# Kernel tuning notes

Measured on AMD Instinct MI355X. Metric: run time of the kernel, lower is better.

Reference implementation:

```python
import jax, jax.numpy as jnp
import numpy as np

B, S, F_IN, E, H, NIT = 256, 196, 384, 384, 8, 10
FH = E                      # hidden_features defaults to embed_dim
EH = E // H                 # embed dim per head = 48
FHH = FH // H               # hidden features per head = 48
OSEQ = S                    # hidden_seq_len defaults to seq_len
MIN_POS = 1e-6
W_THRESH = 1e-5


def _l1(x, axis=-1, eps=1e-12):
    # F.normalize(p=1): x / max(sum|x|, eps)
    return x / jnp.clip(jnp.sum(jnp.abs(x), axis=axis, keepdims=True), eps, None)


def _norm_weight(w):
    # normalize_weights(): L1-normalize, clamp at threshold, L1-normalize again
    w = _l1(w, axis=-1)
    w = jnp.clip(w, W_THRESH, None)
    return _l1(w, axis=-1)


def setup_inputs() -> dict:
    key = jax.random.key(0)
    ks = jax.random.split(key, 7)
    x = jax.random.normal(ks[0], (B, S, F_IN), dtype=jnp.float32)
    # h init: torch.rand in _reset_h (uniform positive)
    h0 = jax.random.uniform(ks[1], (B, OSEQ, H, FHH), dtype=jnp.float32)
    embed_w = jax.random.normal(ks[2], (E, F_IN), dtype=jnp.float32) * 0.05
    embed_b = jnp.zeros((E,), dtype=jnp.float32)
    local_weight = _norm_weight(jax.random.uniform(ks[3], (FHH, EH), dtype=jnp.float32))
    global_weight = _norm_weight(jax.random.uniform(ks[4], (H, OSEQ, S), dtype=jnp.float32))
    out_w = jax.random.normal(ks[5], (F_IN, E), dtype=jnp.float32) * 0.05
    out_b = jnp.zeros((F_IN,), dtype=jnp.float32)
    return {"x": x, "h0": h0, "embed_w": embed_w, "embed_b": embed_b,
            "local_weight": local_weight, "global_weight": global_weight,
            "out_w": out_w, "out_b": out_b}


def reference(x, h0, embed_w, embed_b, local_weight, global_weight, out_w, out_b):
    # embed + clamp + split heads: [B,S,H,EH]
    xe = jnp.clip(x @ embed_w.T + embed_b, MIN_POS, None)
    xe = xe.reshape(B, S, H, EH)
    # _prepare_input: L1 normalize over last dim (eps=1e-20); nonneg so |x|=x
    inp = xe / jnp.clip(jnp.sum(xe, axis=-1, keepdims=True), 1e-20, None)
    # h init, L1-normalized
    h = _l1(h0, axis=-1)

    def nnmf_forward(t):  # t: [B,S(=i),H,EH]
        t = jnp.einsum('bihe,fe->bihf', t, local_weight)          # F.linear(x, local_weight)
        return jnp.einsum('bihf,hoi->bohf', t, global_weight)     # [B,O,H,FHH]

    def nnmf_reconstruct(hh):  # hh: [B,O,H,FHH]
        t = jnp.einsum('bohf,hoi->bihf', hh, global_weight)
        return jnp.einsum('bihf,fe->bihe', t, local_weight)       # F.linear(., local_weight.t())

    # fixed-point NNMF iterations (h_update_rate=1)
    for _ in range(NIT):
        rec = jnp.clip(nnmf_reconstruct(h), MIN_POS, None)   # secure tensor
        rec = _l1(rec, axis=-1)                              # normalize_reconstruction
        h = h * nnmf_forward(inp / rec)                      # multiplicative update
        h = jnp.clip(h, MIN_POS, None)                       # _secure_tensor
        h = h / jnp.sum(h, axis=-1, keepdims=True)           # PowerSoftmax(power=1)

    # output = 'hidden': flatten heads, project back to features
    out = h.reshape(B, OSEQ, FH)
    return out @ out_w.T + out_b
```

## Files before the change

### kernel.cpp

```cpp
#include <hip/hip_runtime.h>
#include <stdint.h>

#define NB   256
#define NS   196
#define NF   384
#define NH   8
#define NEH  48
#define NIT  10
#define SP   224
#define EP   64
#define NBH  2048
#define NBS  50176
#define NT   13

using f32x4  = __attribute__((ext_vector_type(4))) float;
using u16x8  = __attribute__((ext_vector_type(8))) uint16_t;
using u16x4  = __attribute__((ext_vector_type(4))) uint16_t;
using bf16x8 = __attribute__((ext_vector_type(8))) __bf16;

static __device__ __forceinline__ float bf2f(uint16_t u){
  union { uint32_t u32; float f; } c; c.u32 = (uint32_t)u << 16; return c.f;
}
static __device__ __forceinline__ uint16_t f2bf(float f){
  __bf16 h = (__bf16)f;
  return __builtin_bit_cast(uint16_t, h);
}
static __device__ __forceinline__ float frcp(float f){
  return __builtin_amdgcn_rcpf(f);
}
static __device__ __forceinline__ bf16x8 ld8(const uint16_t* p){
  return __builtin_bit_cast(bf16x8, *(const u16x8*)p);
}
static __device__ __forceinline__ void lds_fence(){
  asm volatile("s_waitcnt lgkmcnt(0)" ::: "memory");
}
static __device__ __forceinline__ float dpp_add16(float x){
  int v = __builtin_bit_cast(int, x);
  x += __builtin_bit_cast(float, __builtin_amdgcn_update_dpp(0, v, 0xB1, 0xF, 0xF, false));
  v = __builtin_bit_cast(int, x);
  x += __builtin_bit_cast(float, __builtin_amdgcn_update_dpp(0, v, 0x4E, 0xF, 0xF, false));
  v = __builtin_bit_cast(int, x);
  x += __builtin_bit_cast(float, __builtin_amdgcn_update_dpp(0, v, 0x141, 0xF, 0xF, false));
  v = __builtin_bit_cast(int, x);
  x += __builtin_bit_cast(float, __builtin_amdgcn_update_dpp(0, v, 0x140, 0xF, 0xF, false));
  return x;
}
#define MFMA16(a,b,c) __builtin_amdgcn_mfma_f32_16x16x32_bf16((a),(b),(c),0,0,0)


__global__ void k_prep_gw(const float* __restrict__ gw, uint16_t* __restrict__ gw_b,
                          uint16_t* __restrict__ gwt_b){
  int idx = blockIdx.x * 256 + threadIdx.x;
  if (idx >= NH*SP*SP) return;
  int h = idx / (SP*SP);
  int r = (idx / SP) % SP;
  int c = idx % SP;
  float v = (r < NS && c < NS) ? gw[((size_t)h*NS + r)*NS + c] : 0.f;
  uint16_t bv = f2bf(v);
  gw_b[idx] = bv;
  gwt_b[((size_t)h*SP + c)*SP + r] = bv;
}

__global__ void k_prep_small(const float* __restrict__ lw, const float* __restrict__ ew,
                             const float* __restrict__ ow,
                             uint16_t* __restrict__ lw_b, uint16_t* __restrict__ lwt_b,
                             uint16_t* __restrict__ ew_b, uint16_t* __restrict__ ow_b){
  int idx = blockIdx.x * 256 + threadIdx.x;
  if (idx < EP*EP){
    int f = idx >> 6, e = idx & 63;
    float v = (f < NEH && e < NEH) ? lw[f*NEH + e] : 0.f;
    uint16_t bv = f2bf(v);
    lw_b[f*EP + e] = bv;
    lwt_b[e*EP + f] = bv;
  }
  if (idx < NF*NF){
    ew_b[idx] = f2bf(ew[idx]);
    ow_b[idx] = f2bf(ow[idx]);
  }
}

__global__ __launch_bounds__(512) void k_embed(const float* __restrict__ x,
    const uint16_t* __restrict__ ew_b, const float* __restrict__ eb,
    uint16_t* __restrict__ inp_fm){
  const int wave = threadIdx.x >> 6, lane = threadIdx.x & 63;
  const int lg = lane >> 4, li = lane & 15;
  const int mt = wave >> 1, nh = wave & 1;
  const int m0 = blockIdx.x * 64 + mt * 16;
  f32x4 acc[12];
  #pragma unroll
  for (int i = 0; i < 12; ++i) acc[i] = (f32x4)0.0f;
  const float* ap = x + (size_t)(m0 + li) * NF + 8*lg;
  for (int kt = 0; kt < 12; ++kt){
    f32x4 a0 = *(const f32x4*)(ap + kt*32);
    f32x4 a1 = *(const f32x4*)(ap + kt*32 + 4);
    u16x8 au;
    #pragma unroll
    for (int j = 0; j < 4; ++j){ au[j] = f2bf(a0[j]); au[j+4] = f2bf(a1[j]); }
    bf16x8 a = __builtin_bit_cast(bf16x8, au);
    #pragma unroll
    for (int nt = 0; nt < 12; ++nt){
      bf16x8 b = ld8(ew_b + (size_t)((nh*12 + nt)*16 + li)*NF + kt*32 + 8*lg);
      acc[nt] = MFMA16(a, b, acc[nt]);
    }
  }
  #pragma unroll
  for (int hl = 0; hl < 4; ++hl){
    int hh = nh*4 + hl;
    float xec[3][4];
    float s[4] = {0.f, 0.f, 0.f, 0.f};
    #pragma unroll
    for (int j = 0; j < 3; ++j){
      int nt = hl*3 + j;
      float bias = eb[(nh*12 + nt)*16 + li];
      #pragma unroll
      for (int r = 0; r < 4; ++r){
        float v = fmaxf(acc[nt][r] + bias, 1e-6f);
        xec[j][r] = v; s[r] += v;
      }
    }
    #pragma unroll
    for (int r = 0; r < 4; ++r) s[r] = dpp_add16(s[r]);
    #pragma unroll
    for (int r = 0; r < 4; ++r){
      int m = m0 + 4*lg + r;
      int b = m / NS, si = m - b*NS;
      int t = si >> 4, wi = si & 15;
      int lanep = (wi >> 2)*16 + li;
      float inv = frcp(s[r]);
      size_t base = ((size_t)((b*NH + hh)*NT + t)*64 + lanep)*12 + (wi & 3);
      #pragma unroll
      for (int j = 0; j < 3; ++j)
        inp_fm[base + j*4] = f2bf(xec[j][r] * inv);
    }
  }
}

__global__ __launch_bounds__(448) void k_main(
    const float*    __restrict__ h0,
    const uint16_t* __restrict__ gw_b,
    const uint16_t* __restrict__ gwt_b,
    const uint16_t* __restrict__ lw_b,
    const uint16_t* __restrict__ lwt_b,
    const uint16_t* __restrict__ inp_fm,
    uint16_t* __restrict__ h_b)
{
  __shared__ __align__(16) uint16_t hlT[48][232];
  __shared__ __align__(16) uint16_t t2T[48][232];
  __shared__ __align__(16) uint16_t Sg[7][2][16][72];

  const int bh = blockIdx.x;
  const int b  = bh >> 3;
  const int hh = bh & 7;
  const int tid = threadIdx.x;
  const int wave = tid >> 6;
  const int lane = tid & 63;
  const int lg = lane >> 4;
  const int li = lane & 15;
  const int tt[2] = {wave, wave + 7};

  {
    u16x4 z = {0,0,0,0};
    *(u16x4*)&Sg[wave][0][li][48 + 4*lg] = z;
    *(u16x4*)&Sg[wave][1][li][48 + 4*lg] = z;
  }

  bf16x8 lwtF[3][2], lwF[3][2];
  #pragma unroll
  for (int nt = 0; nt < 3; ++nt)
    #pragma unroll
    for (int kt = 0; kt < 2; ++kt){
      lwtF[nt][kt] = ld8(lwt_b + (size_t)(nt*16 + li)*EP + kt*32 + 8*lg);
      lwF [nt][kt] = ld8(lw_b  + (size_t)(nt*16 + li)*EP + kt*32 + 8*lg);
    }

  u16x4 ip[2][3];
  #pragma unroll
  for (int tp = 0; tp < 2; ++tp){
    const int t = tt[tp];
    if (t < NT){
      const uint16_t* ipp = inp_fm + ((size_t)(bh*NT + t)*64 + lg*16 + li)*12;
      ip[tp][0] = *(const u16x4*)(ipp);
      ip[tp][1] = *(const u16x4*)(ipp + 4);
      ip[tp][2] = *(const u16x4*)(ipp + 8);
    } else {
      u16x4 z = {0,0,0,0};
      ip[tp][0] = z; ip[tp][1] = z; ip[tp][2] = z;
    }
  }

  float hr[2][3][4];
  #pragma unroll
  for (int tp = 0; tp < 2; ++tp){
    const int t = tt[tp];
    float s[4] = {0.f,0.f,0.f,0.f};
    #pragma unroll
    for (int nt = 0; nt < 3; ++nt)
      #pragma unroll
      for (int r = 0; r < 4; ++r){
        int row = t*16 + 4*lg + r;
        float v = 0.f;
        if (row < NS)
          v = h0[(((size_t)(b*NS + row))*NH + hh)*NEH + nt*16 + li];
        hr[tp][nt][r] = v;
        s[r] += fabsf(v);
      }
    #pragma unroll
    for (int r = 0; r < 4; ++r) s[r] = frcp(fmaxf(dpp_add16(s[r]), 1e-12f));
    #pragma unroll
    for (int nt = 0; nt < 3; ++nt)
      #pragma unroll
      for (int r = 0; r < 4; ++r){
        hr[tp][nt][r] *= s[r];
        Sg[wave][tp][4*lg + r][nt*16 + li] = f2bf(hr[tp][nt][r]);
      }
  }
  lds_fence();
  #pragma unroll
  for (int tp = 0; tp < 2; ++tp){
    const int t = tt[tp];
    f32x4 hl[3];
    #pragma unroll
    for (int i = 0; i < 3; ++i) hl[i] = (f32x4)0.0f;
    #pragma unroll
    for (int kt = 0; kt < 2; ++kt){
      bf16x8 a = ld8(&Sg[wave][tp][li][kt*32 + 8*lg]);
      #pragma unroll
      for (int nt = 0; nt < 3; ++nt) hl[nt] = MFMA16(a, lwtF[nt][kt], hl[nt]);
    }
    #pragma unroll
    for (int nt = 0; nt < 3; ++nt){
      u16x4 w;
      #pragma unroll
      for (int r = 0; r < 4; ++r) w[r] = f2bf(hl[nt][r]);
      *(u16x4*)&hlT[nt*16 + li][t*16 + 4*lg] = w;
    }
  }

  const uint16_t* __restrict__ gwh  = gw_b  + (size_t)hh * SP * SP;
  const uint16_t* __restrict__ gwth = gwt_b + (size_t)hh * SP * SP;
  const uint16_t* gA0t = gwth + (size_t)(tt[0]*16 + li)*SP + 8*lg;
  const uint16_t* gA1t = gwth + (size_t)(tt[1]*16 + li)*SP + 8*lg;
  const uint16_t* gA0  = gwh  + (size_t)(tt[0]*16 + li)*SP + 8*lg;
  const uint16_t* gA1  = gwh  + (size_t)(tt[1]*16 + li)*SP + 8*lg;
  __syncthreads();

  for (int it = 0; it < NIT; ++it){
    f32x4 rec[2][3];
    #pragma unroll
    for (int tp = 0; tp < 2; ++tp)
      #pragma unroll
      for (int i = 0; i < 3; ++i) rec[tp][i] = (f32x4)0.0f;
    #pragma unroll
    for (int kt = 0; kt < 7; ++kt){
      bf16x8 b0 = ld8(&hlT[ 0 + li][kt*32 + 8*lg]);
      bf16x8 b1 = ld8(&hlT[16 + li][kt*32 + 8*lg]);
      bf16x8 b2 = ld8(&hlT[32 + li][kt*32 + 8*lg]);
      bf16x8 a0 = ld8(gA0t + kt*32);
      bf16x8 a1 = ld8(gA1t + kt*32);
      rec[0][0] = MFMA16(a0, b0, rec[0][0]);
      rec[0][1] = MFMA16(a0, b1, rec[0][1]);
      rec[0][2] = MFMA16(a0, b2, rec[0][2]);
      rec[1][0] = MFMA16(a1, b0, rec[1][0]);
      rec[1][1] = MFMA16(a1, b1, rec[1][1]);
      rec[1][2] = MFMA16(a1, b2, rec[1][2]);
    }
    #pragma unroll
    for (int tp = 0; tp < 2; ++tp){
      float s[4] = {0.f,0.f,0.f,0.f};
      float rv[3][4];
      #pragma unroll
      for (int nt = 0; nt < 3; ++nt)
        #pragma unroll
        for (int r = 0; r < 4; ++r){
          float v = fmaxf(rec[tp][nt][r], 1e-6f);
          rv[nt][r] = v; s[r] += v;
        }
      #pragma unroll
      for (int r = 0; r < 4; ++r) s[r] = dpp_add16(s[r]);
      #pragma unroll
      for (int r = 0; r < 4; ++r){
        Sg[wave][tp][4*lg + r][ 0 + li] = f2bf(bf2f(ip[tp][0][r]) * s[r] * frcp(rv[0][r]));
        Sg[wave][tp][4*lg + r][16 + li] = f2bf(bf2f(ip[tp][1][r]) * s[r] * frcp(rv[1][r]));
        Sg[wave][tp][4*lg + r][32 + li] = f2bf(bf2f(ip[tp][2][r]) * s[r] * frcp(rv[2][r]));
      }
    }
    lds_fence();
    #pragma unroll
    for (int tp = 0; tp < 2; ++tp){
      const int t = tt[tp];
      f32x4 t2[3];
      #pragma unroll
      for (int i = 0; i < 3; ++i) t2[i] = (f32x4)0.0f;
      #pragma unroll
      for (int kt = 0; kt < 2; ++kt){
        bf16x8 a = ld8(&Sg[wave][tp][li][kt*32 + 8*lg]);
        #pragma unroll
        for (int nt = 0; nt < 3; ++nt) t2[nt] = MFMA16(a, lwF[nt][kt], t2[nt]);
      }
      #pragma unroll
      for (int nt = 0; nt < 3; ++nt){
        u16x4 w;
        #pragma unroll
        for (int r = 0; r < 4; ++r) w[r] = f2bf(t2[nt][r]);
        *(u16x4*)&t2T[nt*16 + li][t*16 + 4*lg] = w;
      }
    }
    __syncthreads();

    f32x4 hu[2][3];
    #pragma unroll
    for (int tp = 0; tp < 2; ++tp)
      #pragma unroll
      for (int i = 0; i < 3; ++i) hu[tp][i] = (f32x4)0.0f;
    #pragma unroll
    for (int kt = 0; kt < 7; ++kt){
      bf16x8 b0 = ld8(&t2T[ 0 + li][kt*32 + 8*lg]);
      bf16x8 b1 = ld8(&t2T[16 + li][kt*32 + 8*lg]);
      bf16x8 b2 = ld8(&t2T[32 + li][kt*32 + 8*lg]);
      bf16x8 a0 = ld8(gA0 + kt*32);
      bf16x8 a1 = ld8(gA1 + kt*32);
      hu[0][0] = MFMA16(a0, b0, hu[0][0]);
      hu[0][1] = MFMA16(a0, b1, hu[0][1]);
      hu[0][2] = MFMA16(a0, b2, hu[0][2]);
      hu[1][0] = MFMA16(a1, b0, hu[1][0]);
      hu[1][1] = MFMA16(a1, b1, hu[1][1]);
      hu[1][2] = MFMA16(a1, b2, hu[1][2]);
    }
    #pragma unroll
    for (int tp = 0; tp < 2; ++tp){
      float s[4] = {0.f,0.f,0.f,0.f};
      #pragma unroll
      for (int nt = 0; nt < 3; ++nt)
        #pragma unroll
        for (int r = 0; r < 4; ++r){
          float v = fmaxf(hr[tp][nt][r] * hu[tp][nt][r], 1e-6f);
          hr[tp][nt][r] = v; s[r] += v;
        }
      #pragma unroll
      for (int r = 0; r < 4; ++r) s[r] = frcp(dpp_add16(s[r]));
      #pragma unroll
      for (int nt = 0; nt < 3; ++nt)
        #pragma unroll
        for (int r = 0; r < 4; ++r){
          hr[tp][nt][r] *= s[r];
          Sg[wave][tp][4*lg + r][nt*16 + li] = f2bf(hr[tp][nt][r]);
        }
    }
    lds_fence();
    #pragma unroll
    for (int tp = 0; tp < 2; ++tp){
      const int t = tt[tp];
      f32x4 hl[3];
      #pragma unroll
      for (int i = 0; i < 3; ++i) hl[i] = (f32x4)0.0f;
      #pragma unroll
      for (int kt = 0; kt < 2; ++kt){
        bf16x8 a = ld8(&Sg[wave][tp][li][kt*32 + 8*lg]);
        #pragma unroll
        for (int nt = 0; nt < 3; ++nt) hl[nt] = MFMA16(a, lwtF[nt][kt], hl[nt]);
      }
      #pragma unroll
      for (int nt = 0; nt < 3; ++nt){
        u16x4 w;
        #pragma unroll
        for (int r = 0; r < 4; ++r) w[r] = f2bf(hl[nt][r]);
        *(u16x4*)&hlT[nt*16 + li][t*16 + 4*lg] = w;
      }
    }
    __syncthreads();
  }

  uint16_t* __restrict__ hrow = h_b + (size_t)bh * SP * EP;
  #pragma unroll
  for (int tp = 0; tp < 2; ++tp){
    const int t = tt[tp];
    #pragma unroll
    for (int nt = 0; nt < 3; ++nt)
      #pragma unroll
      for (int r = 0; r < 4; ++r){
        int row = t*16 + 4*lg + r;
        if (row < NS)
          hrow[(size_t)row*EP + nt*16 + li] = f2bf(hr[tp][nt][r]);
      }
  }
}

__global__ __launch_bounds__(512) void k_out(const uint16_t* __restrict__ h_b,
    const uint16_t* __restrict__ ow_b, const float* __restrict__ obv,
    float* __restrict__ out){
  const int wave = threadIdx.x >> 6, lane = threadIdx.x & 63;
  const int lg = lane >> 4, li = lane & 15;
  const int mt = wave >> 1, nh = wave & 1;
  const int m0 = blockIdx.x * 64 + mt * 16;
  const int m = m0 + li;
  const int b = m / NS, si = m - b*NS;
  f32x4 acc[12];
  #pragma unroll
  for (int i = 0; i < 12; ++i) acc[i] = (f32x4)0.0f;
  for (int kt = 0; kt < 12; ++kt){
    int ks = kt*32 + 8*lg;
    int hh = ks / NEH, f = ks - hh*NEH;
    bf16x8 a = ld8(h_b + ((size_t)(b*NH + hh)*SP + si)*EP + f);
    #pragma unroll
    for (int nt = 0; nt < 12; ++nt){
      bf16x8 bb = ld8(ow_b + (size_t)((nh*12 + nt)*16 + li)*NF + kt*32 + 8*lg);
      acc[nt] = MFMA16(a, bb, acc[nt]);
    }
  }
  #pragma unroll
  for (int nt = 0; nt < 12; ++nt){
    float bias = obv[(nh*12 + nt)*16 + li];
    #pragma unroll
    for (int r = 0; r < 4; ++r)
      out[(size_t)(m0 + 4*lg + r)*NF + (nh*12 + nt)*16 + li] = acc[nt][r] + bias;
  }
}

extern "C" void kernel_launch(void* const* d_in, const int* in_sizes, int n_in,
                              void* d_out, int out_size, void* d_ws, size_t ws_size,
                              hipStream_t stream){
  const float* x   = (const float*)d_in[0];
  const float* h0  = (const float*)d_in[1];
  const float* ew  = (const float*)d_in[2];
  const float* eb  = (const float*)d_in[3];
  const float* lw  = (const float*)d_in[4];
  const float* gw  = (const float*)d_in[5];
  const float* ow  = (const float*)d_in[6];
  const float* obv = (const float*)d_in[7];
  float* out = (float*)d_out;

  char* w = (char*)d_ws;
  size_t o_inp = 0;
  size_t o_hb  = o_inp + (size_t)NBH*NT*64*12*2;
  size_t o_gw  = o_hb  + (size_t)NBH*SP*EP*2;
  size_t o_gwt = o_gw  + (size_t)NH*SP*SP*2;
  size_t o_lw  = o_gwt + (size_t)NH*SP*SP*2;
  size_t o_lwt = o_lw  + (size_t)EP*EP*2;
  size_t o_ew  = o_lwt + (size_t)EP*EP*2;
  size_t o_ow  = o_ew  + (size_t)NF*NF*2;
  size_t total = o_ow  + (size_t)NF*NF*2;
  if (ws_size < total) return;

  uint16_t* inp_fm = (uint16_t*)(w + o_inp);
  uint16_t* h_b    = (uint16_t*)(w + o_hb);
  uint16_t* gw_b   = (uint16_t*)(w + o_gw);
  uint16_t* gwt_b  = (uint16_t*)(w + o_gwt);
  uint16_t* lw_b   = (uint16_t*)(w + o_lw);
  uint16_t* lwt_b  = (uint16_t*)(w + o_lwt);
  uint16_t* ew_b   = (uint16_t*)(w + o_ew);
  uint16_t* ow_b   = (uint16_t*)(w + o_ow);

  k_prep_gw<<<(NH*SP*SP + 255)/256, 256, 0, stream>>>(gw, gw_b, gwt_b);
  k_prep_small<<<(NF*NF + 255)/256, 256, 0, stream>>>(lw, ew, ow, lw_b, lwt_b, ew_b, ow_b);
  k_embed<<<NBS/64, 512, 0, stream>>>(x, ew_b, eb, inp_fm);
  k_main<<<NBH, 448, 0, stream>>>(h0, gw_b, gwt_b, lw_b, lwt_b, inp_fm, h_b);
  k_out<<<NBS/64, 512, 0, stream>>>(h_b, ow_b, obv, out);
}
```

Baseline: 735.4 us.

## Rebalance NNMF tiles across 8 waves, vectorize embed stores, retile output GEMM

The main kernel moves from 7 waves with two tiles each to 8 waves, where waves 0-5 handle two tiles and waves 6-7 handle one, with shared staging indexed by tile. This spreads the 13 tiles over more waves to shorten the per-wave critical path, at the cost of divergent branching on ntile. The embed kernel now hoists the index math and writes four packed bf16 values per store instead of scalar stores. The output GEMM gives each wave two M-tiles by six N-tiles so each B fragment load feeds two MFMAs.

```diff
diff --git a/kernel.cpp b/kernel.cpp
--- a/kernel.cpp
+++ b/kernel.cpp
@@ -103,6 +103,11 @@
       acc[nt] = MFMA16(a, b, acc[nt]);
     }
   }
+  const int mbase = m0 + 4*lg;
+  const int b  = mbase / NS;
+  const int si = mbase - b*NS;
+  const int t  = si >> 4, wi = si & 15;
+  const int lanep = (wi >> 2)*16 + li;
   #pragma unroll
   for (int hl = 0; hl < 4; ++hl){
     int hh = nh*4 + hl;
@@ -119,23 +124,19 @@
       }
     }
     #pragma unroll
-    for (int r = 0; r < 4; ++r) s[r] = dpp_add16(s[r]);
-    #pragma unroll
-    for (int r = 0; r < 4; ++r){
-      int m = m0 + 4*lg + r;
-      int b = m / NS, si = m - b*NS;
-      int t = si >> 4, wi = si & 15;
-      int lanep = (wi >> 2)*16 + li;
-      float inv = frcp(s[r]);
-      size_t base = ((size_t)((b*NH + hh)*NT + t)*64 + lanep)*12 + (wi & 3);
-      #pragma unroll
-      for (int j = 0; j < 3; ++j)
-        inp_fm[base + j*4] = f2bf(xec[j][r] * inv);
-    }
-  }
-}
-
-__global__ __launch_bounds__(448) void k_main(
+    for (int r = 0; r < 4; ++r) s[r] = frcp(dpp_add16(s[r]));
+    uint16_t* dst = inp_fm + ((size_t)((b*NH + hh)*NT + t)*64 + lanep)*12;
+    #pragma unroll
+    for (int j = 0; j < 3; ++j){
+      u16x4 w;
+      #pragma unroll
+      for (int r = 0; r < 4; ++r) w[r] = f2bf(xec[j][r] * s[r]);
+      *(u16x4*)(dst + j*4) = w;
+    }
+  }
+}
+
+__global__ __launch_bounds__(512) void k_main(
     const float*    __restrict__ h0,
     const uint16_t* __restrict__ gw_b,
     const uint16_t* __restrict__ gwt_b,
@@ -146,7 +147,7 @@
 {
   __shared__ __align__(16) uint16_t hlT[48][232];
   __shared__ __align__(16) uint16_t t2T[48][232];
-  __shared__ __align__(16) uint16_t Sg[7][2][16][72];
+  __shared__ __align__(16) uint16_t Sg[14][16][72];
 
   const int bh = blockIdx.x;
   const int b  = bh >> 3;
@@ -156,12 +157,14 @@
   const int lane = tid & 63;
   const int lg = lane >> 4;
   const int li = lane & 15;
-  const int tt[2] = {wave, wave + 7};
+  const int ntile = (wave < 6) ? 2 : 1;
+  const int tt[2] = {wave, wave + 8};
 
   {
     u16x4 z = {0,0,0,0};
-    *(u16x4*)&Sg[wave][0][li][48 + 4*lg] = z;
-    *(u16x4*)&Sg[wave][1][li][48 + 4*lg] = z;
+    #pragma unroll
+    for (int tp = 0; tp < 2; ++tp)
+      if (tp < ntile) *(u16x4*)&Sg[tt[tp]][li][48 + 4*lg] = z;
   }
 
   bf16x8 lwtF[3][2], lwF[3][2];
@@ -176,72 +179,78 @@
   u16x4 ip[2][3];
   #pragma unroll
   for (int tp = 0; tp < 2; ++tp){
-    const int t = tt[tp];
-    if (t < NT){
-      const uint16_t* ipp = inp_fm + ((size_t)(bh*NT + t)*64 + lg*16 + li)*12;
+    u16x4 z = {0,0,0,0};
+    ip[tp][0] = z; ip[tp][1] = z; ip[tp][2] = z;
+    if (tp < ntile && tt[tp] < NT){
+      const uint16_t* ipp = inp_fm + ((size_t)(bh*NT + tt[tp])*64 + lg*16 + li)*12;
       ip[tp][0] = *(const u16x4*)(ipp);
       ip[tp][1] = *(const u16x4*)(ipp + 4);
       ip[tp][2] = *(const u16x4*)(ipp + 8);
-    } else {
-      u16x4 z = {0,0,0,0};
-      ip[tp][0] = z; ip[tp][1] = z; ip[tp][2] = z;
     }
   }
 
   float hr[2][3][4];
   #pragma unroll
   for (int tp = 0; tp < 2; ++tp){
-    const int t = tt[tp];
-    float s[4] = {0.f,0.f,0.f,0.f};
-    #pragma unroll
-    for (int nt = 0; nt < 3; ++nt)
-      #pragma unroll
-      for (int r = 0; r < 4; ++r){
-        int row = t*16 + 4*lg + r;
-        float v = 0.f;
-        if (row < NS)
-          v = h0[(((size_t)(b*NS + row))*NH + hh)*NEH + nt*16 + li];
-        hr[tp][nt][r] = v;
-        s[r] += fabsf(v);
-      }
-    #pragma unroll
-    for (int r = 0; r < 4; ++r) s[r] = frcp(fmaxf(dpp_add16(s[r]), 1e-12f));
-    #pragma unroll
-    for (int nt = 0; nt < 3; ++nt)
-      #pragma unroll
-      for (int r = 0; r < 4; ++r){
-        hr[tp][nt][r] *= s[r];
-        Sg[wave][tp][4*lg + r][nt*16 + li] = f2bf(hr[tp][nt][r]);
-      }
+    if (tp < ntile){
+      const int t = tt[tp];
+      float s[4] = {0.f,0.f,0.f,0.f};
+      #pragma unroll
+      for (int nt = 0; nt < 3; ++nt)
+        #pragma unroll
+        for (int r = 0; r < 4; ++r){
+          int row = t*16 + 4*lg + r;
+          float v = 0.f;
+          if (row < NS)
+            v = h0[(((size_t)(b*NS + row))*NH + hh)*NEH + nt*16 + li];
+          hr[tp][nt][r] = v;
+          s[r] += fabsf(v);
+        }
+      #pragma unroll
+      for (int r = 0; r < 4; ++r) s[r] = frcp(fmaxf(dpp_add16(s[r]), 1e-12f));
+      #pragma unroll
+      for (int nt = 0; nt < 3; ++nt)
+        #pragma unroll
+        for (int r = 0; r < 4; ++r){
+          hr[tp][nt][r] *= s[r];
+          Sg[t][4*lg + r][nt*16 + li] = f2bf(hr[tp][nt][r]);
+        }
+    }
   }
   lds_fence();
   #pragma unroll
   for (int tp = 0; tp < 2; ++tp){
-    const int t = tt[tp];
-    f32x4 hl[3];
-    #pragma unroll
-    for (int i = 0; i < 3; ++i) hl[i] = (f32x4)0.0f;
-    #pragma unroll
-    for (int kt = 0; kt < 2; ++kt){
-      bf16x8 a = ld8(&Sg[wave][tp][li][kt*32 + 8*lg]);
-      #pragma unroll
-      for (int nt = 0; nt < 3; ++nt) hl[nt] = MFMA16(a, lwtF[nt][kt], hl[nt]);
-    }
-    #pragma unroll
-    for (int nt = 0; nt < 3; ++nt){
-      u16x4 w;
-      #pragma unroll
-      for (int r = 0; r < 4; ++r) w[r] = f2bf(hl[nt][r]);
-      *(u16x4*)&hlT[nt*16 + li][t*16 + 4*lg] = w;
+    if (tp < ntile){
+      const int t = tt[tp];
+      f32x4 hl[3];
+      #pragma unroll
+      for (int i = 0; i < 3; ++i) hl[i] = (f32x4)0.0f;
+      #pragma unroll
+      for (int kt = 0; kt < 2; ++kt){
+        bf16x8 a = ld8(&Sg[t][li][kt*32 + 8*lg]);
+        #pragma unroll
+        for (int nt = 0; nt < 3; ++nt) hl[nt] = MFMA16(a, lwtF[nt][kt], hl[nt]);
+      }
+      #pragma unroll
+      for (int nt = 0; nt < 3; ++nt){
+        u16x4 w;
+        #pragma unroll
+        for (int r = 0; r < 4; ++r) w[r] = f2bf(hl[nt][r]);
+        *(u16x4*)&hlT[nt*16 + li][t*16 + 4*lg] = w;
+      }
     }
   }
 
   const uint16_t* __restrict__ gwh  = gw_b  + (size_t)hh * SP * SP;
   const uint16_t* __restrict__ gwth = gwt_b + (size_t)hh * SP * SP;
   const uint16_t* gA0t = gwth + (size_t)(tt[0]*16 + li)*SP + 8*lg;
-  const uint16_t* gA1t = gwth + (size_t)(tt[1]*16 + li)*SP + 8*lg;
+  const uint16_t* gA1t = gwth + (size_t)(tt[0]*16 + li)*SP + 8*lg;
   const uint16_t* gA0  = gwh  + (size_t)(tt[0]*16 + li)*SP + 8*lg;
-  const uint16_t* gA1  = gwh  + (size_t)(tt[1]*16 + li)*SP + 8*lg;
+  const uint16_t* gA1  = gA0;
+  if (ntile == 2){
+    gA1t = gwth + (size_t)(tt[1]*16 + li)*SP + 8*lg;
+    gA1  = gwh  + (size_t)(tt[1]*16 + li)*SP + 8*lg;
+  }
   __syncthreads();
 
   for (int it = 0; it < NIT; ++it){
@@ -256,53 +265,60 @@
       bf16x8 b1 = ld8(&hlT[16 + li][kt*32 + 8*lg]);
       bf16x8 b2 = ld8(&hlT[32 + li][kt*32 + 8*lg]);
       bf16x8 a0 = ld8(gA0t + kt*32);
-      bf16x8 a1 = ld8(gA1t + kt*32);
       rec[0][0] = MFMA16(a0, b0, rec[0][0]);
       rec[0][1] = MFMA16(a0, b1, rec[0][1]);
       rec[0][2] = MFMA16(a0, b2, rec[0][2]);
-      rec[1][0] = MFMA16(a1, b0, rec[1][0]);
-      rec[1][1] = MFMA16(a1, b1, rec[1][1]);
-      rec[1][2] = MFMA16(a1, b2, rec[1][2]);
+      if (ntile == 2){
+        bf16x8 a1 = ld8(gA1t + kt*32);
+        rec[1][0] = MFMA16(a1, b0, rec[1][0]);
+        rec[1][1] = MFMA16(a1, b1, rec[1][1]);
+        rec[1][2] = MFMA16(a1, b2, rec[1][2]);
+      }
     }
     #pragma unroll
     for (int tp = 0; tp < 2; ++tp){
-      float s[4] = {0.f,0.f,0.f,0.f};
-      float rv[3][4];
-      #pragma unroll
-      for (int nt = 0; nt < 3; ++nt)
+      if (tp < ntile){
+        const int t = tt[tp];
+        float s[4] = {0.f,0.f,0.f,0.f};
+        float rv[3][4];
+        #pragma unroll
+        for (int nt = 0; nt < 3; ++nt)
+          #pragma unroll
+          for (int r = 0; r < 4; ++r){
+            float v = fmaxf(rec[tp][nt][r], 1e-6f);
+            rv[nt][r] = v; s[r] += v;
+          }
+        #pragma unroll
+        for (int r = 0; r < 4; ++r) s[r] = dpp_add16(s[r]);
         #pragma unroll
         for (int r = 0; r < 4; ++r){
-          float v = fmaxf(rec[tp][nt][r], 1e-6f);
-          rv[nt][r] = v; s[r] += v;
-        }
-      #pragma unroll
-      for (int r = 0; r < 4; ++r) s[r] = dpp_add16(s[r]);
-      #pragma unroll
-      for (int r = 0; r < 4; ++r){
-        Sg[wave][tp][4*lg + r][ 0 + li] = f2bf(bf2f(ip[tp][0][r]) * s[r] * frcp(rv[0][r]));
-        Sg[wave][tp][4*lg + r][16 + li] = f2bf(bf2f(ip[tp][1][r]) * s[r] * frcp(rv[1][r]));
-        Sg[wave][tp][4*lg + r][32 + li] = f2bf(bf2f(ip[tp][2][r]) * s[r] * frcp(rv[2][r]));
+          Sg[t][4*lg + r][ 0 + li] = f2bf(bf2f(ip[tp][0][r]) * s[r] * frcp(rv[0][r]));
+          Sg[t][4*lg + r][16 + li] = f2bf(bf2f(ip[tp][1][r]) * s[r] * frcp(rv[1][r]));
+          Sg[t][4*lg + r][32 + li] = f2bf(bf2f(ip[tp][2][r]) * s[r] * frcp(rv[2][r]));
+        }
       }
     }
     lds_fence();
     #pragma unroll
     for (int tp = 0; tp < 2; ++tp){
-      const int t = tt[tp];
-      f32x4 t2[3];
-      #pragma unroll
-      for (int i = 0; i < 3; ++i) t2[i] = (f32x4)0.0f;
-      #pragma unroll
-      for (int kt = 0; kt < 2; ++kt){
-        bf16x8 a = ld8(&Sg[wave][tp][li][kt*32 + 8*lg]);
-        #pragma unroll
-        for (int nt = 0; nt < 3; ++nt) t2[nt] = MFMA16(a, lwF[nt][kt], t2[nt]);
-      }
-      #pragma unroll
-      for (int nt = 0; nt < 3; ++nt){
-        u16x4 w;
-        #pragma unroll
-        for (int r = 0; r < 4; ++r) w[r] = f2bf(t2[nt][r]);
-        *(u16x4*)&t2T[nt*16 + li][t*16 + 4*lg] = w;
+      if (tp < ntile){
+        const int t = tt[tp];
+        f32x4 t2[3];
+        #pragma unroll
+        for (int i = 0; i < 3; ++i) t2[i] = (f32x4)0.0f;
+        #pragma unroll
+        for (int kt = 0; kt < 2; ++kt){
+          bf16x8 a = ld8(&Sg[t][li][kt*32 + 8*lg]);
+          #pragma unroll
+          for (int nt = 0; nt < 3; ++nt) t2[nt] = MFMA16(a, lwF[nt][kt], t2[nt]);
+        }
+        #pragma unroll
+        for (int nt = 0; nt < 3; ++nt){
+          u16x4 w;
+          #pragma unroll
+          for (int r = 0; r < 4; ++r) w[r] = f2bf(t2[nt][r]);
+          *(u16x4*)&t2T[nt*16 + li][t*16 + 4*lg] = w;
+        }
       }
     }
     __syncthreads();
@@ -318,70 +334,79 @@
       bf16x8 b1 = ld8(&t2T[16 + li][kt*32 + 8*lg]);
       bf16x8 b2 = ld8(&t2T[32 + li][kt*32 + 8*lg]);
       bf16x8 a0 = ld8(gA0 + kt*32);
-      bf16x8 a1 = ld8(gA1 + kt*32);
       hu[0][0] = MFMA16(a0, b0, hu[0][0]);
       hu[0][1] = MFMA16(a0, b1, hu[0][1]);
       hu[0][2] = MFMA16(a0, b2, hu[0][2]);
-      hu[1][0] = MFMA16(a1, b0, hu[1][0]);
-      hu[1][1] = MFMA16(a1, b1, hu[1][1]);
-      hu[1][2] = MFMA16(a1, b2, hu[1][2]);
+      if (ntile == 2){
+        bf16x8 a1 = ld8(gA1 + kt*32);
+        hu[1][0] = MFMA16(a1, b0, hu[1][0]);
+        hu[1][1] = MFMA16(a1, b1, hu[1][1]);
+        hu[1][2] = MFMA16(a1, b2, hu[1][2]);
+      }
     }
     #pragma unroll
     for (int tp = 0; tp < 2; ++tp){
-      float s[4] = {0.f,0.f,0.f,0.f};
+      if (tp < ntile){
+        const int t = tt[tp];
+        float s[4] = {0.f,0.f,0.f,0.f};
+        #pragma unroll
+        for (int nt = 0; nt < 3; ++nt)
+          #pragma unroll
+          for (int r = 0; r < 4; ++r){
+            float v = fmaxf(hr[tp][nt][r] * hu[tp][nt][r], 1e-6f);
+            hr[tp][nt][r] = v; s[r] += v;
+          }
+        #pragma unroll
+        for (int r = 0; r < 4; ++r) s[r] = frcp(dpp_add16(s[r]));
+        #pragma unroll
+        for (int nt = 0; nt < 3; ++nt)
+          #pragma unroll
+          for (int r = 0; r < 4; ++r){
+            hr[tp][nt][r] *= s[r];
+            Sg[t][4*lg + r][nt*16 + li] = f2bf(hr[tp][nt][r]);
+          }
+      }
+    }
+    lds_fence();
+    #pragma unroll
+    for (int tp = 0; tp < 2; ++tp){
+      if (tp < ntile){
+        const int t = tt[tp];
+        f32x4 hl[3];
+        #pragma unroll
+        for (int i = 0; i < 3; ++i) hl[i] = (f32x4)0.0f;
+        #pragma unroll
+        for (int kt = 0; kt < 2; ++kt){
+          bf16x8 a = ld8(&Sg[t][li][kt*32 + 8*lg]);
+          #pragma unroll
+          for (int nt = 0; nt < 3; ++nt) hl[nt] = MFMA16(a, lwtF[nt][kt], hl[nt]);
+        }
+        #pragma unroll
+        for (int nt = 0; nt < 3; ++nt){
+          u16x4 w;
+          #pragma unroll
+          for (int r = 0; r < 4; ++r) w[r] = f2bf(hl[nt][r]);
+          *(u16x4*)&hlT[nt*16 + li][t*16 + 4*lg] = w;
+        }
+      }
+    }
+    __syncthreads();
+  }
+
+  uint16_t* __restrict__ hrow = h_b + (size_t)bh * SP * EP;
+  #pragma unroll
+  for (int tp = 0; tp < 2; ++tp){
+    if (tp < ntile){
+      const int t = tt[tp];
       #pragma unroll
       for (int nt = 0; nt < 3; ++nt)
         #pragma unroll
         for (int r = 0; r < 4; ++r){
-          float v = fmaxf(hr[tp][nt][r] * hu[tp][nt][r], 1e-6f);
-          hr[tp][nt][r] = v; s[r] += v;
-        }
-      #pragma unroll
-      for (int r = 0; r < 4; ++r) s[r] = frcp(dpp_add16(s[r]));
-      #pragma unroll
-      for (int nt = 0; nt < 3; ++nt)
-        #pragma unroll
-        for (int r = 0; r < 4; ++r){
-          hr[tp][nt][r] *= s[r];
-          Sg[wave][tp][4*lg + r][nt*16 + li] = f2bf(hr[tp][nt][r]);
-        }
-    }
-    lds_fence();
-    #pragma unroll
-    for (int tp = 0; tp < 2; ++tp){
-      const int t = tt[tp];
-      f32x4 hl[3];
-      #pragma unroll
-      for (int i = 0; i < 3; ++i) hl[i] = (f32x4)0.0f;
-      #pragma unroll
-      for (int kt = 0; kt < 2; ++kt){
-        bf16x8 a = ld8(&Sg[wave][tp][li][kt*32 + 8*lg]);
-        #pragma unroll
-        for (int nt = 0; nt < 3; ++nt) hl[nt] = MFMA16(a, lwtF[nt][kt], hl[nt]);
-      }
-      #pragma unroll
-      for (int nt = 0; nt < 3; ++nt){
-        u16x4 w;
-        #pragma unroll
-        for (int r = 0; r < 4; ++r) w[r] = f2bf(hl[nt][r]);
-        *(u16x4*)&hlT[nt*16 + li][t*16 + 4*lg] = w;
-      }
-    }
-    __syncthreads();
-  }
-
-  uint16_t* __restrict__ hrow = h_b + (size_t)bh * SP * EP;
-  #pragma unroll
-  for (int tp = 0; tp < 2; ++tp){
-    const int t = tt[tp];
-    #pragma unroll
-    for (int nt = 0; nt < 3; ++nt)
-      #pragma unroll
-      for (int r = 0; r < 4; ++r){
-        int row = t*16 + 4*lg + r;
-        if (row < NS)
-          hrow[(size_t)row*EP + nt*16 + li] = f2bf(hr[tp][nt][r]);
-      }
+          int row = t*16 + 4*lg + r;
+          if (row < NS)
+            hrow[(size_t)row*EP + nt*16 + li] = f2bf(hr[tp][nt][r]);
+        }
+    }
   }
 }
 
@@ -390,29 +415,43 @@
     float* __restrict__ out){
   const int wave = threadIdx.x >> 6, lane = threadIdx.x & 63;
   const int lg = lane >> 4, li = lane & 15;
-  const int mt = wave >> 1, nh = wave & 1;
-  const int m0 = blockIdx.x * 64 + mt * 16;
-  const int m = m0 + li;
-  const int b = m / NS, si = m - b*NS;
-  f32x4 acc[12];
-  #pragma unroll
-  for (int i = 0; i < 12; ++i) acc[i] = (f32x4)0.0f;
+  const int p = wave >> 2, q = wave & 3;
+  const int m0 = blockIdx.x * 64;
+  f32x4 acc[2][6];
+  #pragma unroll
+  for (int mtl = 0; mtl < 2; ++mtl)
+    #pragma unroll
+    for (int i = 0; i < 6; ++i) acc[mtl][i] = (f32x4)0.0f;
+  size_t rowbase[2];
+  #pragma unroll
+  for (int mtl = 0; mtl < 2; ++mtl){
+    int m = m0 + (2*p + mtl)*16 + li;
+    int b = m / NS, si = m - b*NS;
+    rowbase[mtl] = ((size_t)b*NH*SP + si)*EP;
+  }
   for (int kt = 0; kt < 12; ++kt){
     int ks = kt*32 + 8*lg;
     int hh = ks / NEH, f = ks - hh*NEH;
-    bf16x8 a = ld8(h_b + ((size_t)(b*NH + hh)*SP + si)*EP + f);
-    #pragma unroll
-    for (int nt = 0; nt < 12; ++nt){
-      bf16x8 bb = ld8(ow_b + (size_t)((nh*12 + nt)*16 + li)*NF + kt*32 + 8*lg);
-      acc[nt] = MFMA16(a, bb, acc[nt]);
-    }
-  }
-  #pragma unroll
-  for (int nt = 0; nt < 12; ++nt){
-    float bias = obv[(nh*12 + nt)*16 + li];
-    #pragma unroll
-    for (int r = 0; r < 4; ++r)
-      out[(size_t)(m0 + 4*lg + r)*NF + (nh*12 + nt)*16 + li] = acc[nt][r] + bias;
+    size_t koff = (size_t)hh*SP*EP + f;
+    bf16x8 a0 = ld8(h_b + rowbase[0] + koff);
+    bf16x8 a1 = ld8(h_b + rowbase[1] + koff);
+    #pragma unroll
+    for (int n = 0; n < 6; ++n){
+      bf16x8 bb = ld8(ow_b + (size_t)((6*q + n)*16 + li)*NF + kt*32 + 8*lg);
+      acc[0][n] = MFMA16(a0, bb, acc[0][n]);
+      acc[1][n] = MFMA16(a1, bb, acc[1][n]);
+    }
+  }
+  #pragma unroll
+  for (int mtl = 0; mtl < 2; ++mtl){
+    #pragma unroll
+    for (int n = 0; n < 6; ++n){
+      int col = (6*q + n)*16 + li;
+      float bias = obv[col];
+      #pragma unroll
+      for (int r = 0; r < 4; ++r)
+        out[(size_t)(m0 + (2*p + mtl)*16 + 4*lg + r)*NF + col] = acc[mtl][n][r] + bias;
+    }
   }
 }
 
@@ -453,6 +492,6 @@
   k_prep_gw<<<(NH*SP*SP + 255)/256, 256, 0, stream>>>(gw, gw_b, gwt_b);
   k_prep_small<<<(NF*NF + 255)/256, 256, 0, stream>>>(lw, ew, ow, lw_b, lwt_b, ew_b, ow_b);
   k_embed<<<NBS/64, 512, 0, stream>>>(x, ew_b, eb, inp_fm);
-  k_main<<<NBH, 448, 0, stream>>>(h0, gw_b, gwt_b, lw_b, lwt_b, inp_fm, h_b);
+  k_main<<<NBH, 512, 0, stream>>>(h0, gw_b, gwt_b, lw_b, lwt_b, inp_fm, h_b);
   k_out<<<NBS/64, 512, 0, stream>>>(h_b, ow_b, obv, out);
 }
```

Result: slower. 754.8 us (+2.6%).
